# Kernel optimization log

Measured on AMD Instinct MI355X. Metric: run time of the kernel, lower is better.

Reference implementation:

```python
import jax, jax.numpy as jnp
import numpy as np

NUM_CLASSES = 41


def conv3x3(x, w):
    # x: [B,Cin,H,W], w: [Cout,Cin,3,3], padding=1, bias=False
    return jax.lax.conv_general_dilated(
        x, w, window_strides=(1, 1), padding=((1, 1), (1, 1)),
        dimension_numbers=("NCHW", "OIHW", "NCHW"))


def ra_module(feats, labels_ds, w1, w2, key):
    """RA: per-(batch,label) segment-mean of features, replacing the
    original nested python loops with one fused segment_sum.
    feats: [b,c,h,w]; labels_ds: [b,h,w] int; w1: [c//16,c]; w2: [c,c//16]."""
    b, c, h, w = feats.shape
    n = h * w
    f = feats.reshape(b, c, n).transpose(0, 2, 1).reshape(b * n, c)  # [b*n, c]
    seg = (jnp.arange(b, dtype=jnp.int32)[:, None] * NUM_CLASSES
           + labels_ds.reshape(b, n)).reshape(-1)                    # [b*n]
    sums = jax.ops.segment_sum(f, seg, num_segments=b * NUM_CLASSES)
    cnt = jax.ops.segment_sum(jnp.ones((b * n,), f.dtype), seg,
                              num_segments=b * NUM_CLASSES)
    mean = sums / jnp.maximum(cnt, 1.0)[:, None]
    # torch code initializes the queue with randn and only overwrites
    # classes present in the label map; absent classes keep random values.
    init = jax.random.normal(key, (b * NUM_CLASSES, c), dtype=f.dtype)
    queue = jnp.where((cnt > 0)[:, None], mean, init).reshape(b, NUM_CLASSES, c)
    # F.normalize(att, dim=1): L2-normalize across the class dimension
    att = queue / jnp.maximum(
        jnp.linalg.norm(queue, axis=1, keepdims=True), 1e-12)
    att = att.sum(axis=1)                                            # [b, c]
    hid = jax.nn.relu(att @ w1.T)                                    # 1x1 conv on 1x1 map == matmul
    out = jax.nn.sigmoid(hid @ w2.T)                                 # [b, c]
    return out[:, :, None, None]


def setup_inputs() -> dict:
    key = jax.random.key(0)
    ks = jax.random.split(key, 8)
    B, C, H, W = 4, 128, 224, 224
    r = jax.random.normal(ks[0], (B, C, H, W), dtype=jnp.float32)
    d = jax.random.normal(ks[1], (B, C, H, W), dtype=jnp.float32)
    label = jax.random.randint(ks[2], (B, 4 * H, 4 * W), 0, NUM_CLASSES,
                               dtype=jnp.int32)
    w_fuse = jax.random.normal(ks[3], (C, 2 * C, 3, 3), dtype=jnp.float32) * 0.02
    w1_d = jax.random.normal(ks[4], (C // 16, C), dtype=jnp.float32) * 0.1
    w2_d = jax.random.normal(ks[5], (C, C // 16), dtype=jnp.float32) * 0.1
    w1_f = jax.random.normal(ks[6], (C // 16, C), dtype=jnp.float32) * 0.1
    w2_f = jax.random.normal(ks[7], (C, C // 16), dtype=jnp.float32) * 0.1
    return {"r": r, "d": d, "label": label, "w_fuse": w_fuse,
            "w1_d": w1_d, "w2_d": w2_d, "w1_f": w1_f, "w2_f": w2_f}


def reference(r, d, label, w_fuse, w1_d, w2_d, w1_f, w2_f):
    # nearest-neighbor downsample of labels to feature resolution
    # (exact integer ratio 4 -> strided slice, matches torch 'nearest')
    labels_ds = label[:, ::4, ::4]
    add = r + d
    mul = r * jax.nn.sigmoid(d)
    fuse = conv3x3(jnp.concatenate([add, mul], axis=1), w_fuse)
    d_ra = d * ra_module(d, labels_ds, w1_d, w2_d, jax.random.key(1))
    fuse_ra = fuse * ra_module(fuse, labels_ds, w1_f, w2_f, jax.random.key(2))
    return fuse_ra + d_ra
```

## Files before the change

kernel.cpp:

```cpp
#include <hip/hip_runtime.h>
#include <hip/hip_bf16.h>
#include <cstdint>
#include <cstddef>

typedef unsigned short u16;
typedef unsigned int   u32;
typedef unsigned char  u8;

#define NCLS 41

typedef short s16x8 __attribute__((ext_vector_type(8)));
typedef float f32x4 __attribute__((ext_vector_type(4)));

__device__ __forceinline__ u16 f2bf(float f) {
  u32 u = __float_as_uint(f);
  u += 0x7fffu + ((u >> 16) & 1u);
  return (u16)(u >> 16);
}

#if __has_builtin(__builtin_amdgcn_global_load_lds)
#define HAVE_GLL 1
typedef const __attribute__((address_space(1))) u32* gas1p;
typedef __attribute__((address_space(3))) u32* las3p;
__device__ __forceinline__ void gll16(const void* g, void* l) {
  __builtin_amdgcn_global_load_lds((gas1p)g, (las3p)l, 16, 0, 0);
}
#else
#define HAVE_GLL 0
#endif

__global__ void k_wprep(const float* __restrict__ wf, u16* __restrict__ Wt) {
  const int e = blockIdx.x * 256 + threadIdx.x;
  if (e >= 9 * 128 * 256) return;
  const int tap = e / (128 * 256);
  const int oc  = (e / 256) % 128;
  const int ic  = e % 256;
  Wt[e] = f2bf(wf[((size_t)oc * 256 + ic) * 9 + tap]);
}

__global__ void k_labels(const int* __restrict__ label, u8* __restrict__ labs,
                         int* __restrict__ counts) {
  const int i = blockIdx.x % 224, b = blockIdx.x / 224;
  __shared__ int hist[NCLS];
  const int t = threadIdx.x;
  if (t < NCLS) hist[t] = 0;
  __syncthreads();
  if (t < 224) {
    const int v = label[((size_t)b * 896 + 4 * i) * 896 + 4 * t];
    labs[((size_t)b * 224 + i) * 224 + t] = (u8)v;
    atomicAdd(&hist[v], 1);
  }
  __syncthreads();
  if (t < NCLS) atomicAdd(&counts[b * NCLS + t], hist[t]);
}

__global__ __launch_bounds__(256) void k_prep(const float* __restrict__ r,
                                              const float* __restrict__ d,
                                              const u8* __restrict__ labs,
                                              u16* __restrict__ X,
                                              float* __restrict__ sums_d) {
  const int t  = threadIdx.x;
  const int yp = blockIdx.x % 226;
  const int b  = blockIdx.x / 226;
  u32* Xrow = (u32*)(X + (size_t)(b * 226 + yp) * 226 * 256);
  if (yp == 0 || yp == 225) {
    for (int e = t; e < 226 * 128; e += 256) Xrow[e] = 0u;
    return;
  }
  const int y = yp - 1;
  if (t < 128) Xrow[t] = 0u;
  else         Xrow[225 * 128 + (t - 128)] = 0u;

  __shared__ float lA[16 * 225];
  __shared__ float lM[16 * 225];
  __shared__ float acc[NCLS * 129];
  __shared__ u8 ll[224];
  for (int e = t; e < NCLS * 129; e += 256) acc[e] = 0.f;
  if (t < 224) ll[t] = labs[((size_t)b * 224 + y) * 224 + t];

  const float* rb = r + (size_t)b * 128 * 50176 + y * 224;
  const float* db = d + (size_t)b * 128 * 50176 + y * 224;
  for (int c0 = 0; c0 < 128; c0 += 16) {
    __syncthreads();
    for (int e = t; e < 16 * 224; e += 256) {
      const int c = e / 224, x = e % 224;
      const float rv = rb[(size_t)(c0 + c) * 50176 + x];
      const float dv = db[(size_t)(c0 + c) * 50176 + x];
      lA[c * 225 + x] = rv + dv;
      lM[c * 225 + x] = rv / (1.f + __expf(-dv));
      atomicAdd(&acc[(int)ll[x] * 129 + (c0 + c)], dv);
    }
    __syncthreads();
    for (int e = t; e < 224 * 8; e += 256) {
      const int px = e / 8, j = e % 8, cj = 2 * j;
      u32 a0 = (u32)f2bf(lA[cj * 225 + px]) | ((u32)f2bf(lA[(cj + 1) * 225 + px]) << 16);
      u32 m0 = (u32)f2bf(lM[cj * 225 + px]) | ((u32)f2bf(lM[(cj + 1) * 225 + px]) << 16);
      Xrow[(px + 1) * 128 +      (c0 >> 1) + j] = a0;
      Xrow[(px + 1) * 128 + 64 + (c0 >> 1) + j] = m0;
    }
  }
  __syncthreads();
  for (int e = t; e < NCLS * 128; e += 256)
    atomicAdd(&sums_d[b * NCLS * 128 + e], acc[(e / 128) * 129 + (e % 128)]);
}

__global__ __launch_bounds__(256) void k_conv(const u16* __restrict__ X,
                                              const u16* __restrict__ Wt,
                                              u16* __restrict__ fuse) {
  __shared__ u16 Alds[128 * 32];
  __shared__ u16 Blds[128 * 32];
  const int t = threadIdx.x;
  const int w = t >> 6, l = t & 63;
  const int lrow = l & 15, lq = l >> 4;
  const int wm = (w & 1) * 64, wn = (w >> 1) * 64;

  const int L   = blockIdx.x;
  const int xcd = L & 7;
  const int i   = L >> 3;
  const int b   = i / 56;
  const int rem = i % 56;
  const int y   = xcd * 28 + (rem >> 1);
  const int x0  = (rem & 1) * 128;

  f32x4 acc[4][4] = {};

  const int posA = t >> 2;
  const int koff = (t & 3) * 8;
  char* ldsA0 = (char*)Alds + (w * 64) * 16;
  char* ldsB0 = (char*)Blds + (w * 64) * 16;

  for (int tap = 0; tap < 9; ++tap) {
    const int dy = tap / 3, dx = tap % 3;
    const u16* Abase = X + ((size_t)((b * 226 + y + dy) * 226) + (x0 + dx)) * 256;
    const u16* Bbase = Wt + (size_t)tap * (128 * 256);
    for (int s = 0; s < 8; ++s) {
      const int kb = s * 32;
      const u16* ga0 = Abase + (size_t)posA * 256 + kb + koff;
      const u16* gb0 = Bbase + (size_t)posA * 256 + kb + koff;
#if HAVE_GLL
      gll16(ga0, ldsA0);
      gll16(gb0, ldsB0);
      gll16(ga0 + 64 * 256, ldsA0 + 256 * 16);
      gll16(gb0 + 64 * 256, ldsB0 + 256 * 16);
#else
      *(uint4*)((char*)Alds + (size_t)t * 16)         = *(const uint4*)ga0;
      *(uint4*)((char*)Blds + (size_t)t * 16)         = *(const uint4*)gb0;
      *(uint4*)((char*)Alds + (size_t)(256 + t) * 16) = *(const uint4*)(ga0 + 64 * 256);
      *(uint4*)((char*)Blds + (size_t)(256 + t) * 16) = *(const uint4*)(gb0 + 64 * 256);
#endif
      __syncthreads();
      s16x8 af[4], bfr[4];
#pragma unroll
      for (int mi = 0; mi < 4; ++mi)
        af[mi] = *(const s16x8*)((const char*)Alds + (wm + mi * 16 + lrow) * 64 + lq * 16);
#pragma unroll
      for (int ni = 0; ni < 4; ++ni)
        bfr[ni] = *(const s16x8*)((const char*)Blds + (wn + ni * 16 + lrow) * 64 + lq * 16);
#pragma unroll
      for (int mi = 0; mi < 4; ++mi)
#pragma unroll
        for (int ni = 0; ni < 4; ++ni)
          acc[mi][ni] = __builtin_amdgcn_mfma_f32_16x16x32_bf16(af[mi], bfr[ni], acc[mi][ni], 0, 0, 0);
      __syncthreads();
    }
  }
#pragma unroll
  for (int mi = 0; mi < 4; ++mi) {
#pragma unroll
    for (int rr = 0; rr < 4; ++rr) {
      const int pos = wm + mi * 16 + lq * 4 + rr;
      const int x = x0 + pos;
      if (x < 224) {
        u16* dst = fuse + ((size_t)(b * 224 + y) * 224 + x) * 128;
#pragma unroll
        for (int ni = 0; ni < 4; ++ni) {
          const int oc = wn + ni * 16 + lrow;
          dst[oc] = f2bf(acc[mi][ni][rr]);
        }
      }
    }
  }
}

__global__ __launch_bounds__(256) void k_segf(const u16* __restrict__ fuse,
                                              const u8* __restrict__ labs,
                                              float* __restrict__ sums_f) {
  const int y = blockIdx.x % 224, b = blockIdx.x / 224;
  __shared__ float acc[NCLS * 129];
  __shared__ u8 ll[224];
  const int t = threadIdx.x;
  for (int e = t; e < NCLS * 129; e += 256) acc[e] = 0.f;
  if (t < 224) ll[t] = labs[((size_t)b * 224 + y) * 224 + t];
  __syncthreads();
  const u32* fb = (const u32*)(fuse + ((size_t)b * 224 + y) * 224 * 128);
  for (int e = t; e < 224 * 64; e += 256) {
    const int c2 = e % 64, px = e / 64;
    const u32 v = fb[(size_t)px * 64 + c2];
    const int lab = ll[px];
    atomicAdd(&acc[lab * 129 + 2 * c2],     __uint_as_float(v << 16));
    atomicAdd(&acc[lab * 129 + 2 * c2 + 1], __uint_as_float(v & 0xffff0000u));
  }
  __syncthreads();
  for (int e = t; e < NCLS * 128; e += 256)
    atomicAdd(&sums_f[b * NCLS * 128 + e], acc[(e / 128) * 129 + (e % 128)]);
}

__global__ __launch_bounds__(256) void k_gates(const float* __restrict__ sums,
                                               const int* __restrict__ counts,
                                               const float* __restrict__ w1,
                                               const float* __restrict__ w2,
                                               float* __restrict__ gates) {
  const int b = blockIdx.x;
  __shared__ float att[128];
  __shared__ float hid[8];
  const int t = threadIdx.x;
  if (t < 128) {
    float s1 = 0.f, s2 = 0.f;
    for (int lb = 0; lb < NCLS; ++lb) {
      const float cnt = (float)counts[b * NCLS + lb];
      const float m = sums[(size_t)b * NCLS * 128 + lb * 128 + t] / fmaxf(cnt, 1.f);
      s1 += m; s2 += m * m;
    }
    att[t] = s1 / fmaxf(sqrtf(s2), 1e-12f);
  }
  __syncthreads();
  if (t < 8) {
    float h = 0.f;
    for (int c = 0; c < 128; ++c) h += att[c] * w1[t * 128 + c];
    hid[t] = fmaxf(h, 0.f);
  }
  __syncthreads();
  if (t < 128) {
    float o = 0.f;
    for (int j = 0; j < 8; ++j) o += hid[j] * w2[t * 8 + j];
    gates[b * 128 + t] = 1.f / (1.f + expf(-o));
  }
}

__global__ __launch_bounds__(256) void k_out(const u16* __restrict__ fuse,
                                             const float* __restrict__ d,
                                             const float* __restrict__ gates,
                                             float* __restrict__ out) {
  const int y = blockIdx.x % 224, b = blockIdx.x / 224;
  __shared__ float flds[224 * 33];
  __shared__ float gf[128], gd[128];
  const int t = threadIdx.x;
  if (t < 128) gd[t] = gates[b * 128 + t];
  else         gf[t - 128] = gates[512 + b * 128 + (t - 128)];
  const u32* frow = (const u32*)fuse + ((size_t)b * 224 + y) * 224 * 64;
  const float* db = d + (size_t)b * 128 * 50176 + y * 224;
  float* ob = out + (size_t)b * 128 * 50176 + y * 224;
  for (int c0 = 0; c0 < 128; c0 += 32) {
    __syncthreads();
    for (int e = t; e < 224 * 16; e += 256) {
      const int px = e / 16, q = e % 16;
      const u32 v = frow[(size_t)px * 64 + (c0 >> 1) + q];
      flds[px * 33 + 2 * q]     = __uint_as_float(v << 16);
      flds[px * 33 + 2 * q + 1] = __uint_as_float(v & 0xffff0000u);
    }
    __syncthreads();
    for (int e = t; e < 32 * 224; e += 256) {
      const int cc = e / 224, x = e % 224, c = c0 + cc;
      ob[(size_t)c * 50176 + x] = flds[x * 33 + cc] * gf[c] + db[(size_t)c * 50176 + x] * gd[c];
    }
  }
}

extern "C" void kernel_launch(void* const* d_in, const int* in_sizes, int n_in,
                              void* d_out, int out_size, void* d_ws, size_t ws_size,
                              hipStream_t stream) {
  const float* r     = (const float*)d_in[0];
  const float* d     = (const float*)d_in[1];
  const int*   label = (const int*)d_in[2];
  const float* wf    = (const float*)d_in[3];
  const float* w1d   = (const float*)d_in[4];
  const float* w2d   = (const float*)d_in[5];
  const float* w1f   = (const float*)d_in[6];
  const float* w2f   = (const float*)d_in[7];
  float* out = (float*)d_out;

  char* ws = (char*)d_ws;
  size_t off = 0;
  auto carve = [&](size_t bytes) -> char* {
    char* p = ws + off;
    off = (off + bytes + 511) & ~(size_t)511;
    return p;
  };
  u16* X       = (u16*)carve((size_t)4 * 226 * 226 * 256 * 2 + 65536);
  u16* Wt      = (u16*)carve((size_t)9 * 128 * 256 * 2);
  u16* fuseb   = (u16*)carve((size_t)4 * 224 * 224 * 128 * 2);
  u8*  labs    = (u8*) carve((size_t)4 * 224 * 224);
  int* counts  = (int*)carve(4 * NCLS * sizeof(int));
  float* sumsd = (float*)carve((size_t)4 * NCLS * 128 * 4);
  float* sumsf = (float*)carve((size_t)4 * NCLS * 128 * 4);
  float* gates = (float*)carve(1024 * sizeof(float));

  hipMemsetAsync(counts, 0, 4 * NCLS * sizeof(int), stream);
  hipMemsetAsync(sumsd, 0, (size_t)4 * NCLS * 128 * 4, stream);
  hipMemsetAsync(sumsf, 0, (size_t)4 * NCLS * 128 * 4, stream);
  k_wprep <<<(9 * 128 * 256 + 255) / 256, 256, 0, stream>>>(wf, Wt);
  k_labels<<<4 * 224, 256, 0, stream>>>(label, labs, counts);
  k_prep  <<<4 * 226, 256, 0, stream>>>(r, d, labs, X, sumsd);
  k_conv  <<<1792, 256, 0, stream>>>(X, Wt, fuseb);
  k_segf  <<<4 * 224, 256, 0, stream>>>(fuseb, labs, sumsf);
  k_gates <<<4, 256, 0, stream>>>(sumsd, counts, w1d, w2d, gates);
  k_gates <<<4, 256, 0, stream>>>(sumsf, counts, w1f, w2f, gates + 512);
  k_out   <<<4 * 224, 256, 0, stream>>>(fuseb, d, gates, out);
}
```

Measured before the change: 868.6 us.

## Replace global atomic segment sums with per-row partials and a reduction kernel

```diff
diff --git a/kernel.cpp b/kernel.cpp
--- a/kernel.cpp
+++ b/kernel.cpp
@@ -58,7 +58,7 @@
                                               const float* __restrict__ d,
                                               const u8* __restrict__ labs,
                                               u16* __restrict__ X,
-                                              float* __restrict__ sums_d) {
+                                              float* __restrict__ partd) {
   const int t  = threadIdx.x;
   const int yp = blockIdx.x % 226;
   const int b  = blockIdx.x / 226;
@@ -100,8 +100,9 @@
     }
   }
   __syncthreads();
+  float* pb = partd + (size_t)(b * 224 + y) * NCLS * 128;
   for (int e = t; e < NCLS * 128; e += 256)
-    atomicAdd(&sums_d[b * NCLS * 128 + e], acc[(e / 128) * 129 + (e % 128)]);
+    pb[e] = acc[(e / 128) * 129 + (e % 128)];
 }
 
 __global__ __launch_bounds__(256) void k_conv(const u16* __restrict__ X,
@@ -184,7 +185,7 @@
 
 __global__ __launch_bounds__(256) void k_segf(const u16* __restrict__ fuse,
                                               const u8* __restrict__ labs,
-                                              float* __restrict__ sums_f) {
+                                              float* __restrict__ partf) {
   const int y = blockIdx.x % 224, b = blockIdx.x / 224;
   __shared__ float acc[NCLS * 129];
   __shared__ u8 ll[224];
@@ -201,12 +202,29 @@
     atomicAdd(&acc[lab * 129 + 2 * c2 + 1], __uint_as_float(v & 0xffff0000u));
   }
   __syncthreads();
+  float* pb = partf + (size_t)(b * 224 + y) * NCLS * 128;
   for (int e = t; e < NCLS * 128; e += 256)
-    atomicAdd(&sums_f[b * NCLS * 128 + e], acc[(e / 128) * 129 + (e % 128)]);
-}
-
-__global__ __launch_bounds__(256) void k_gates(const float* __restrict__ sums,
-                                               const int* __restrict__ counts,
+    pb[e] = acc[(e / 128) * 129 + (e % 128)];
+}
+
+__global__ __launch_bounds__(256) void k_reduce(const float* __restrict__ part,
+                                                const int* __restrict__ counts,
+                                                float* __restrict__ mean) {
+  const int lab = blockIdx.x, b = blockIdx.y;
+  const int c = threadIdx.x & 127, h = threadIdx.x >> 7;
+  __shared__ float buf[2][128];
+  float s = 0.f;
+  const float* p = part + (((size_t)(b * 224 + h * 112)) * NCLS + lab) * 128 + c;
+  for (int y = 0; y < 112; ++y) s += p[(size_t)y * NCLS * 128];
+  buf[h][c] = s;
+  __syncthreads();
+  if (threadIdx.x < 128) {
+    const float cnt = (float)counts[b * NCLS + lab];
+    mean[((size_t)b * NCLS + lab) * 128 + c] = (buf[0][c] + buf[1][c]) / fmaxf(cnt, 1.f);
+  }
+}
+
+__global__ __launch_bounds__(256) void k_gates(const float* __restrict__ mean,
                                                const float* __restrict__ w1,
                                                const float* __restrict__ w2,
                                                float* __restrict__ gates) {
@@ -217,8 +235,7 @@
   if (t < 128) {
     float s1 = 0.f, s2 = 0.f;
     for (int lb = 0; lb < NCLS; ++lb) {
-      const float cnt = (float)counts[b * NCLS + lb];
-      const float m = sums[(size_t)b * NCLS * 128 + lb * 128 + t] / fmaxf(cnt, 1.f);
+      const float m = mean[((size_t)b * NCLS + lb) * 128 + t];
       s1 += m; s2 += m * m;
     }
     att[t] = s1 / fmaxf(sqrtf(s2), 1e-12f);
@@ -291,19 +308,21 @@
   u16* fuseb   = (u16*)carve((size_t)4 * 224 * 224 * 128 * 2);
   u8*  labs    = (u8*) carve((size_t)4 * 224 * 224);
   int* counts  = (int*)carve(4 * NCLS * sizeof(int));
-  float* sumsd = (float*)carve((size_t)4 * NCLS * 128 * 4);
-  float* sumsf = (float*)carve((size_t)4 * NCLS * 128 * 4);
+  float* partd = (float*)carve((size_t)4 * 224 * NCLS * 128 * 4);
+  float* partf = (float*)carve((size_t)4 * 224 * NCLS * 128 * 4);
+  float* meand = (float*)carve((size_t)4 * NCLS * 128 * 4);
+  float* meanf = (float*)carve((size_t)4 * NCLS * 128 * 4);
   float* gates = (float*)carve(1024 * sizeof(float));
 
   hipMemsetAsync(counts, 0, 4 * NCLS * sizeof(int), stream);
-  hipMemsetAsync(sumsd, 0, (size_t)4 * NCLS * 128 * 4, stream);
-  hipMemsetAsync(sumsf, 0, (size_t)4 * NCLS * 128 * 4, stream);
   k_wprep <<<(9 * 128 * 256 + 255) / 256, 256, 0, stream>>>(wf, Wt);
   k_labels<<<4 * 224, 256, 0, stream>>>(label, labs, counts);
-  k_prep  <<<4 * 226, 256, 0, stream>>>(r, d, labs, X, sumsd);
+  k_prep  <<<4 * 226, 256, 0, stream>>>(r, d, labs, X, partd);
   k_conv  <<<1792, 256, 0, stream>>>(X, Wt, fuseb);
-  k_segf  <<<4 * 224, 256, 0, stream>>>(fuseb, labs, sumsf);
-  k_gates <<<4, 256, 0, stream>>>(sumsd, counts, w1d, w2d, gates);
-  k_gates <<<4, 256, 0, stream>>>(sumsf, counts, w1f, w2f, gates + 512);
+  k_segf  <<<4 * 224, 256, 0, stream>>>(fuseb, labs, partf);
+  k_reduce<<<dim3(NCLS, 4), 256, 0, stream>>>(partd, counts, meand);
+  k_reduce<<<dim3(NCLS, 4), 256, 0, stream>>>(partf, counts, meanf);
+  k_gates <<<4, 256, 0, stream>>>(meand, w1d, w2d, gates);
+  k_gates <<<4, 256, 0, stream>>>(meanf, w1f, w2f, gates + 512);
   k_out   <<<4 * 224, 256, 0, stream>>>(fuseb, d, gates, out);
 }
```

Result: no change. 873.1 us (+0.5%).
